# Kernel tuning notes

Hardware: AMD Instinct MI355X
Metric: run time of the kernel (lower is better)

Reference implementation:

```python
import jax, jax.numpy as jnp
import numpy as np

NHEAD, DK, DV, DMODEL, L = 8, 64, 64, 512, 32

def setup_inputs() -> dict:
    key = jax.random.key(0)
    ks = jax.random.split(key, 9)
    B, N = 4, 2048
    s = 1.0 / np.sqrt(DMODEL)
    return {
        "q": jax.random.normal(ks[0], (B, N, DMODEL), jnp.float32),
        "k": jax.random.normal(ks[1], (B, N, DMODEL), jnp.float32),
        "v": jax.random.normal(ks[2], (B, N, DMODEL), jnp.float32),
        "Wq": jax.random.normal(ks[3], (DMODEL, NHEAD * DK), jnp.float32) * s,
        "Wk": jax.random.normal(ks[4], (DMODEL, NHEAD * DK), jnp.float32) * s,
        "Wv": jax.random.normal(ks[5], (DMODEL, NHEAD * DV), jnp.float32) * s,
        "Wfc": jax.random.normal(ks[6], (NHEAD * DV, DMODEL), jnp.float32) * s,
        "ln_g": jnp.ones((DMODEL,), jnp.float32),
        "ln_b": jnp.zeros((DMODEL,), jnp.float32),
    }

def reference(q, k, v, Wq, Wk, Wv, Wfc, ln_g, ln_b):
    B, Nq, _ = q.shape
    residual = q
    # project and split heads: [B, H, N, d]
    qh = (q @ Wq).reshape(B, Nq, NHEAD, DK).transpose(0, 2, 1, 3)
    kh = (k @ Wk).reshape(B, k.shape[1], NHEAD, DK).transpose(0, 2, 1, 3)
    vh = (v @ Wv).reshape(B, v.shape[1], NHEAD, DV).transpose(0, 2, 1, 3)
    # scaled dot-product scores and softmax over keys
    attn = jnp.einsum('bhqd,bhkd->bhqk', qh / jnp.sqrt(jnp.float32(DK)), kh)
    attn = jax.nn.softmax(attn, axis=-1)
    # AWG: keep entries >= l-th largest per row, renormalize
    threshold = jax.lax.top_k(attn, L)[0][..., -1:]  # [B,H,Nq,1]
    W = jnp.where(attn >= threshold, attn, 0.0)
    W_out = W / jnp.sum(W, axis=-1, keepdims=True)
    out = jnp.einsum('bhqk,bhkd->bhqd', W_out, vh)
    out = out.transpose(0, 2, 1, 3).reshape(B, Nq, NHEAD * DV)
    out = out @ Wfc + residual
    # LayerNorm, eps=1e-6
    mu = jnp.mean(out, axis=-1, keepdims=True)
    var = jnp.var(out, axis=-1, keepdims=True)
    return (out - mu) / jnp.sqrt(var + 1e-6) * ln_g + ln_b
```

## Files before the change

### kernel.cpp

```cpp
#include <hip/hip_runtime.h>
#include <hip/hip_fp16.h>

#define BATCH 4
#define NSEQ 2048
#define DMODEL 512
#define NHEAD 8
#define HDIM 64
#define LSEL 32
#define SROWU 2056
#define MAXL 128
#define QROWS 8

typedef __attribute__((ext_vector_type(8))) _Float16 f16x8;
typedef __attribute__((ext_vector_type(4))) float f32x4;

__device__ inline ushort f2h(float x) { __half h = __float2half(x); return *reinterpret_cast<ushort*>(&h); }
__device__ inline uint h2sort(ushort h) { return (h & 0x8000u) ? (uint)(h ^ 0xFFFFu) : (uint)(h | 0x8000u); }
__device__ inline float sort2f(uint su) {
    ushort hb = (su & 0x8000u) ? (ushort)(su ^ 0x8000u) : (ushort)(su ^ 0xFFFFu);
    __half th; *reinterpret_cast<ushort*>(&th) = hb;
    return __half2float(th);
}

__global__ __launch_bounds__(256) void cvtW_kernel(
    const float* __restrict__ Wq, const float* __restrict__ Wk,
    const float* __restrict__ Wv, const float* __restrict__ Wfc,
    ushort* __restrict__ Wt)
{
    const int z = blockIdx.y;
    const float* W = (z == 0) ? Wq : (z == 1) ? Wk : (z == 2) ? Wv : Wfc;
    ushort* O = Wt + (size_t)z * DMODEL * DMODEL;
    const int gt = blockIdx.x * 256 + threadIdx.x;
    const int n = gt & 511;
    const int kc = (gt >> 9) * 16;
    uint pk[8];
#pragma unroll
    for (int i = 0; i < 8; ++i) {
        uint lo = f2h(W[(size_t)(kc + 2 * i) * DMODEL + n]);
        uint hi = f2h(W[(size_t)(kc + 2 * i + 1) * DMODEL + n]);
        pk[i] = lo | (hi << 16);
    }
    uint4 u0 = {pk[0], pk[1], pk[2], pk[3]};
    uint4 u1 = {pk[4], pk[5], pk[6], pk[7]};
    *(uint4*)(O + (size_t)n * DMODEL + kc) = u0;
    *(uint4*)(O + (size_t)n * DMODEL + kc + 8) = u1;
}

template<int MODE>
__global__ __launch_bounds__(256, 2) void hgemm_kernel(
    const float* __restrict__ Fq, const float* __restrict__ Fk, const float* __restrict__ Fv,
    const ushort* __restrict__ A16,
    const ushort* __restrict__ Wt,
    ushort* __restrict__ O0, ushort* __restrict__ O1, ushort* __restrict__ O2,
    float* __restrict__ Ofc)
{
    __shared__ ushort Ah[64][40];
    __shared__ ushort Bh[512][40];

    const int tid = threadIdx.x;
    const int wave = tid >> 6, lane = tid & 63;
    const int lr = lane & 15, lg = lane >> 4;
    const int bm = blockIdx.x * 64;
    const int z = blockIdx.y;

    const float* Af = (MODE == 0) ? (z == 0 ? Fq : z == 1 ? Fk : Fv) : nullptr;
    const ushort* Wz = Wt + (size_t)((MODE == 0) ? z : 3) * (DMODEL * DMODEL);

    f32x4 acc[4][8];
#pragma unroll
    for (int i = 0; i < 4; ++i)
#pragma unroll
        for (int j = 0; j < 8; ++j) acc[i][j] = (f32x4){0.f, 0.f, 0.f, 0.f};

    const int sar = tid >> 2, sak = (tid & 3) * 8;

    for (int k0 = 0; k0 < DMODEL; k0 += 32) {
        __syncthreads();
        if (MODE == 0) {
            float4 fa = *(const float4*)(Af + (size_t)(bm + sar) * DMODEL + k0 + sak);
            float4 fb = *(const float4*)(Af + (size_t)(bm + sar) * DMODEL + k0 + sak + 4);
            uint4 pk;
            pk.x = (uint)f2h(fa.x) | ((uint)f2h(fa.y) << 16);
            pk.y = (uint)f2h(fa.z) | ((uint)f2h(fa.w) << 16);
            pk.z = (uint)f2h(fb.x) | ((uint)f2h(fb.y) << 16);
            pk.w = (uint)f2h(fb.z) | ((uint)f2h(fb.w) << 16);
            *(uint4*)&Ah[sar][sak] = pk;
        } else {
            *(uint4*)&Ah[sar][sak] = *(const uint4*)(A16 + (size_t)(bm + sar) * DMODEL + k0 + sak);
        }
#pragma unroll
        for (int i = 0; i < 8; ++i) {
            int n = sar + 64 * i;
            *(uint4*)&Bh[n][sak] = *(const uint4*)(Wz + (size_t)n * DMODEL + k0 + sak);
        }
        __syncthreads();
        f16x8 af[4];
#pragma unroll
        for (int fr = 0; fr < 4; ++fr) af[fr] = *(const f16x8*)&Ah[fr * 16 + lr][lg * 8];
#pragma unroll
        for (int fc2 = 0; fc2 < 8; ++fc2) {
            f16x8 bf = *(const f16x8*)&Bh[wave * 128 + fc2 * 16 + lr][lg * 8];
#pragma unroll
            for (int fr = 0; fr < 4; ++fr)
                acc[fr][fc2] = __builtin_amdgcn_mfma_f32_16x16x32_f16(af[fr], bf, acc[fr][fc2], 0, 0, 0);
        }
    }

    if (MODE == 1) {
#pragma unroll
        for (int fr = 0; fr < 4; ++fr)
#pragma unroll
            for (int fc2 = 0; fc2 < 8; ++fc2)
#pragma unroll
                for (int r = 0; r < 4; ++r)
                    Ofc[(size_t)(bm + fr * 16 + lg * 4 + r) * DMODEL + wave * 128 + fc2 * 16 + lr] = acc[fr][fc2][r];
        return;
    }

    ushort* O = (z == 0) ? O0 : (z == 1) ? O1 : O2;
    const int b = bm >> 11;
    const int nseq0 = bm & (NSEQ - 1);
    ushort* smw = (ushort*)&Bh[0][0] + wave * (64 * 72);
#pragma unroll
    for (int hp = 0; hp < 2; ++hp) {
        __syncthreads();
#pragma unroll
        for (int f4 = 0; f4 < 4; ++f4) {
            int fc2 = hp * 4 + f4;
            int nl = f4 * 16 + lr;
#pragma unroll
            for (int fr = 0; fr < 4; ++fr)
#pragma unroll
                for (int r = 0; r < 4; ++r)
                    smw[(fr * 16 + lg * 4 + r) * 72 + nl] = f2h(acc[fr][fc2][r]);
        }
        __syncthreads();
        const int h = wave * 2 + hp;
        ushort* obase = O + ((size_t)(b * NHEAD + h) * NSEQ + nseq0) * HDIM;
#pragma unroll
        for (int i = 0; i < 8; ++i) {
            int m = i * 8 + (lane >> 3);
            int dc = (lane & 7) * 8;
            *(uint4*)(obase + (size_t)m * HDIM + dc) = *(const uint4*)(smw + m * 72 + dc);
        }
    }
}

__device__ inline int wave_sum6(int c) {
    int tot = (int)__popcll(__ballot(c & 1));
    tot += (int)__popcll(__ballot(c & 2)) << 1;
    tot += (int)__popcll(__ballot(c & 4)) << 2;
    tot += (int)__popcll(__ballot(c & 8)) << 3;
    tot += (int)__popcll(__ballot(c & 16)) << 4;
    tot += (int)__popcll(__ballot(c & 32)) << 5;
    return tot;
}

__device__ uint full_thr(const ushort* Sr, int lane, uint lo0) {
    uint flo = lo0, fhi = 0xFFFFu;
#pragma unroll 1
    for (int it2 = 0; it2 < 16; ++it2) {
        uint mid = (flo + fhi + 1) >> 1, M = mid << 16;
        int cl = 0;
#pragma unroll
        for (int it = 0; it < 4; ++it) {
            uint4 r4 = *(const uint4*)(Sr + it * 512 + lane * 8);
            cl += ((r4.x << 16) >= M) + ((r4.x & 0xFFFF0000u) >= M);
            cl += ((r4.y << 16) >= M) + ((r4.y & 0xFFFF0000u) >= M);
            cl += ((r4.z << 16) >= M) + ((r4.z & 0xFFFF0000u) >= M);
            cl += ((r4.w << 16) >= M) + ((r4.w & 0xFFFF0000u) >= M);
        }
        bool ge = wave_sum6(cl) >= LSEL;
        flo = ge ? mid : flo;
        fhi = ge ? fhi : mid - 1;
    }
    return flo;
}

__device__ int recount(const ushort* Sr, int lane, uint th) {
    int cs = 0;
#pragma unroll
    for (int it = 0; it < 4; ++it) {
        uint4 r4 = *(const uint4*)(Sr + it * 512 + lane * 8);
        cs += ((r4.x << 16) >= th) + ((r4.x & 0xFFFF0000u) >= th);
        cs += ((r4.y << 16) >= th) + ((r4.y & 0xFFFF0000u) >= th);
        cs += ((r4.z << 16) >= th) + ((r4.z & 0xFFFF0000u) >= th);
        cs += ((r4.w << 16) >= th) + ((r4.w & 0xFFFF0000u) >= th);
    }
    return cs;
}

__device__ float extract_big(const ushort* Sr, int lane, uint th, float Mv,
                             int pre, ushort* li, float* lwp)
{
    const float L2E = 1.4426950408889634f;
    float wp = 0.f;
    int pos = pre;
#pragma unroll
    for (int it = 0; it < 4; ++it) {
        uint4 r4 = *(const uint4*)(Sr + it * 512 + lane * 8);
        uint ib = (uint)(it * 512 + lane * 8);
        uint wds[4] = {r4.x, r4.y, r4.z, r4.w};
#pragma unroll
        for (int c = 0; c < 4; ++c) {
            uint vL = wds[c] << 16, vH = wds[c] & 0xFFFF0000u;
            if (vL >= th) {
                float w = exp2f((sort2f(vL >> 16) - Mv) * L2E);
                if (pos < MAXL) { li[pos] = (ushort)(ib + c * 2); lwp[pos] = w; wp += w; }
                ++pos;
            }
            if (vH >= th) {
                float w = exp2f((sort2f(vH >> 16) - Mv) * L2E);
                if (pos < MAXL) { li[pos] = (ushort)(ib + c * 2 + 1); lwp[pos] = w; wp += w; }
                ++pos;
            }
        }
    }
#pragma unroll
    for (int off = 32; off >= 1; off >>= 1) wp += __shfl_xor(wp, off);
    return wp;
}

__device__ float extract_fast(uint t0, uint t1, uint t2, uint t3,
                              uint th, float Mv, int pre, ushort* li, float* lwp)
{
    const float L2E = 1.4426950408889634f;
    float wp = 0.f;
    uint tt[4] = {t0, t1, t2, t3};
#pragma unroll
    for (int i = 0; i < 4; ++i) {
        if (tt[i] >= th) {
            int pos = pre + i;
            float w = exp2f((sort2f(tt[i] >> 16) - Mv) * L2E);
            if (pos < MAXL) { li[pos] = (ushort)(tt[i] & 0xFFFFu); lwp[pos] = w; wp += w; }
        }
    }
#pragma unroll
    for (int off = 32; off >= 1; off >>= 1) wp += __shfl_xor(wp, off);
    return wp;
}

#define INS5(T0, T1, T2, T3, T4, P) { \
    uint m1_ = min(P, T0); T0 = max(P, T0); \
    uint m2_ = min(m1_, T1); T1 = max(m1_, T1); \
    uint m3_ = min(m2_, T2); T2 = max(m2_, T2); \
    uint m4_ = min(m3_, T3); T3 = max(m3_, T3); \
    T4 = max(m4_, T4); }

__global__ __launch_bounds__(512, 8) void attn_kernel(
    const ushort* __restrict__ qh, const ushort* __restrict__ kh,
    const ushort* __restrict__ vh, ushort* __restrict__ ao)
{
    __shared__ __align__(16) ushort Sbuf[QROWS * SROWU];
    __shared__ ushort lidx[QROWS][MAXL];
    __shared__ float  lw[QROWS][MAXL];

    const int tid = threadIdx.x;
    const int wave = tid >> 6;
    const int lane = tid & 63;
    const int bh = blockIdx.y;
    const int q0 = blockIdx.x * QROWS;
    const int lr = lane & 15;
    const int lg = lane >> 4;

    const ushort* Qb = qh + ((size_t)bh * NSEQ + q0) * HDIM;
    const ushort* Kb = kh + (size_t)bh * NSEQ * HDIM;

    f16x8 qf0 = *(const f16x8*)(Qb + (lr & 7) * HDIM + lg * 8);
    f16x8 qf1 = *(const f16x8*)(Qb + (lr & 7) * HDIM + 32 + lg * 8);

    for (int t = 0; t < 16; ++t) {
        const int k0 = wave * 256 + t * 16;
        const ushort* Kt = Kb + (size_t)k0 * HDIM;
        f16x8 a0 = *(const f16x8*)(Kt + lr * HDIM + lg * 8);
        f16x8 a1 = *(const f16x8*)(Kt + lr * HDIM + 32 + lg * 8);
        f32x4 acc = {0.f, 0.f, 0.f, 0.f};
        acc = __builtin_amdgcn_mfma_f32_16x16x32_f16(a0, qf0, acc, 0, 0, 0);
        acc = __builtin_amdgcn_mfma_f32_16x16x32_f16(a1, qf1, acc, 0, 0, 0);
        if (lr < QROWS) {
            uint2 pk;
            pk.x = h2sort(f2h(acc[0] * 0.125f)) | (h2sort(f2h(acc[1] * 0.125f)) << 16);
            pk.y = h2sort(f2h(acc[2] * 0.125f)) | (h2sort(f2h(acc[3] * 0.125f)) << 16);
            *(uint2*)&Sbuf[lr * SROWU + k0 + lg * 4] = pk;
        }
    }
    __syncthreads();

    const ushort* Vb = vh + (size_t)bh * NSEQ * HDIM;
    const int b = bh >> 3, hh = bh & 7;
    const unsigned long long below = (1ULL << lane) - 1ULL;

    const int qr = wave;
    const ushort* Sr = &Sbuf[qr * SROWU];

    uint a0 = 0, a1 = 0, a2 = 0, a3 = 0, a4 = 0;
#pragma unroll
    for (int it = 0; it < 4; ++it) {
        uint4 ra = *(const uint4*)(Sr + it * 512 + lane * 8);
        uint ib = (uint)(it * 512 + lane * 8);
        uint p;
        p = (ra.x << 16) | (ib + 0); INS5(a0, a1, a2, a3, a4, p);
        p = (ra.x & 0xFFFF0000u) | (ib + 1); INS5(a0, a1, a2, a3, a4, p);
        p = (ra.y << 16) | (ib + 2); INS5(a0, a1, a2, a3, a4, p);
        p = (ra.y & 0xFFFF0000u) | (ib + 3); INS5(a0, a1, a2, a3, a4, p);
        p = (ra.z << 16) | (ib + 4); INS5(a0, a1, a2, a3, a4, p);
        p = (ra.z & 0xFFFF0000u) | (ib + 5); INS5(a0, a1, a2, a3, a4, p);
        p = (ra.w << 16) | (ib + 6); INS5(a0, a1, a2, a3, a4, p);
        p = (ra.w & 0xFFFF0000u) | (ib + 7); INS5(a0, a1, a2, a3, a4, p);
    }

    uint mx = a0;
#pragma unroll
    for (int off = 32; off >= 1; off >>= 1) mx = max(mx, (uint)__shfl_xor((int)mx, off));
    const float Mv = sort2f(mx >> 16);

    uint lo = 0, hi = 0xFFFFu;
#pragma unroll
    for (int it = 0; it < 16; ++it) {
        uint mid = (lo + hi + 1) >> 1, M = mid << 16;
        int c = (a0 >= M) + (a1 >= M) + (a2 >= M) + (a3 >= M);
        int tot = (int)__popcll(__ballot(c & 1)) + ((int)__popcll(__ballot(c & 2)) << 1)
                + ((int)__popcll(__ballot(c & 4)) << 2);
        bool ge = tot >= LSEL;
        lo = ge ? mid : lo;
        hi = ge ? hi : mid - 1;
    }
    uint th = lo << 16;

    const bool miss = __any(a4 >= th);

    int csel;
    if (!miss) {
        csel = (a0 >= th) + (a1 >= th) + (a2 >= th) + (a3 >= th);
    } else {
        int cgt = recount(Sr, lane, th + 0x10000u);
        if (wave_sum6(cgt) >= LSEL) { lo = full_thr(Sr, lane, lo); th = lo << 16; }
        csel = recount(Sr, lane, th);
    }

    int pre = 0, totsel = 0;
#pragma unroll
    for (int bb = 0; bb < 6; ++bb) {
        unsigned long long m = __ballot((csel >> bb) & 1);
        pre += (int)__popcll(m & below) << bb;
        totsel += (int)__popcll(m) << bb;
    }

    const float wsum = miss
        ? extract_big(Sr, lane, th, Mv, pre, &lidx[qr][0], &lw[qr][0])
        : extract_fast(a0, a1, a2, a3, th, Mv, pre, &lidx[qr][0], &lw[qr][0]);

    const int nk = (totsel < MAXL) ? totsel : MAXL;

    asm volatile("s_waitcnt lgkmcnt(0)" ::: "memory");

    const int half = lane >> 5;
    const int dp = lane & 31;
    const __half2* V2 = reinterpret_cast<const __half2*>(Vb);

    float ox = 0.f, oy = 0.f;
    int j = half;
    for (; j + 6 < nk; j += 8) {
        int i0 = lidx[qr][j + 0]; float w0 = lw[qr][j + 0];
        int i1 = lidx[qr][j + 2]; float w1 = lw[qr][j + 2];
        int i2 = lidx[qr][j + 4]; float w2 = lw[qr][j + 4];
        int i3 = lidx[qr][j + 6]; float w3 = lw[qr][j + 6];
        float2 v0 = __half22float2(V2[(size_t)i0 * 32 + dp]);
        float2 v1 = __half22float2(V2[(size_t)i1 * 32 + dp]);
        float2 v2 = __half22float2(V2[(size_t)i2 * 32 + dp]);
        float2 v3 = __half22float2(V2[(size_t)i3 * 32 + dp]);
        ox += w0 * v0.x + w1 * v1.x + w2 * v2.x + w3 * v3.x;
        oy += w0 * v0.y + w1 * v1.y + w2 * v2.y + w3 * v3.y;
    }
    for (; j < nk; j += 2) {
        int i0 = lidx[qr][j]; float w0 = lw[qr][j];
        float2 v0 = __half22float2(V2[(size_t)i0 * 32 + dp]);
        ox += w0 * v0.x; oy += w0 * v0.y;
    }
    ox += __shfl_xor(ox, 32);
    oy += __shfl_xor(oy, 32);

    if (half == 0) {
        const float inv = 1.f / wsum;
        uint opk = (uint)f2h(ox * inv) | ((uint)f2h(oy * inv) << 16);
        *(uint*)(ao + ((size_t)(b * NSEQ) + q0 + qr) * DMODEL + hh * HDIM + dp * 2) = opk;
    }
}

__global__ __launch_bounds__(256) void ln_kernel(
    const float* __restrict__ fcr, const float* __restrict__ resid,
    const float* __restrict__ g, const float* __restrict__ bta, float* __restrict__ out)
{
    const int row = blockIdx.x * 4 + (threadIdx.x >> 6);
    const int lane = threadIdx.x & 63;
    const size_t base = (size_t)row * DMODEL + lane * 8;
    float4 xa = *(const float4*)(fcr + base);
    float4 xb = *(const float4*)(fcr + base + 4);
    float4 ra = *(const float4*)(resid + base);
    float4 rb = *(const float4*)(resid + base + 4);
    xa.x += ra.x; xa.y += ra.y; xa.z += ra.z; xa.w += ra.w;
    xb.x += rb.x; xb.y += rb.y; xb.z += rb.z; xb.w += rb.w;
    float sum = xa.x + xa.y + xa.z + xa.w + xb.x + xb.y + xb.z + xb.w;
    float sq = xa.x * xa.x + xa.y * xa.y + xa.z * xa.z + xa.w * xa.w
             + xb.x * xb.x + xb.y * xb.y + xb.z * xb.z + xb.w * xb.w;
#pragma unroll
    for (int off = 32; off >= 1; off >>= 1) {
        sum += __shfl_xor(sum, off);
        sq += __shfl_xor(sq, off);
    }
    float mean = sum * (1.f / 512.f);
    float var = sq * (1.f / 512.f) - mean * mean;
    float rstd = rsqrtf(var + 1e-6f);
    float4 ga = *(const float4*)(g + lane * 8);
    float4 gb = *(const float4*)(g + lane * 8 + 4);
    float4 ba = *(const float4*)(bta + lane * 8);
    float4 bb = *(const float4*)(bta + lane * 8 + 4);
    float4 oa, ob;
    oa.x = (xa.x - mean) * rstd * ga.x + ba.x;
    oa.y = (xa.y - mean) * rstd * ga.y + ba.y;
    oa.z = (xa.z - mean) * rstd * ga.z + ba.z;
    oa.w = (xa.w - mean) * rstd * ga.w + ba.w;
    ob.x = (xb.x - mean) * rstd * gb.x + bb.x;
    ob.y = (xb.y - mean) * rstd * gb.y + bb.y;
    ob.z = (xb.z - mean) * rstd * gb.z + bb.z;
    ob.w = (xb.w - mean) * rstd * gb.w + bb.w;
    *(float4*)(out + base) = oa;
    *(float4*)(out + base + 4) = ob;
}

extern "C" void kernel_launch(void* const* d_in, const int* in_sizes, int n_in,
                              void* d_out, int out_size, void* d_ws, size_t ws_size,
                              hipStream_t stream)
{
    (void)in_sizes; (void)n_in; (void)out_size; (void)ws_size;

    const float* q   = (const float*)d_in[0];
    const float* k   = (const float*)d_in[1];
    const float* v   = (const float*)d_in[2];
    const float* Wq  = (const float*)d_in[3];
    const float* Wk  = (const float*)d_in[4];
    const float* Wv  = (const float*)d_in[5];
    const float* Wfc = (const float*)d_in[6];
    const float* g   = (const float*)d_in[7];
    const float* b   = (const float*)d_in[8];
    float* out = (float*)d_out;

    const size_t SZ = (size_t)BATCH * NSEQ * DMODEL;
    const size_t WSZ = (size_t)DMODEL * DMODEL;
    ushort* Wt = (ushort*)d_ws;
    ushort* qh = Wt + 4 * WSZ;
    ushort* kh = qh + SZ;
    ushort* vh = kh + SZ;
    ushort* ao = vh + SZ;
    float* fc_raw = (float*)qh;

    cvtW_kernel<<<dim3(64, 4), 256, 0, stream>>>(Wq, Wk, Wv, Wfc, Wt);
    hgemm_kernel<0><<<dim3(128, 3), 256, 0, stream>>>(q, k, v, nullptr, Wt, qh, kh, vh, nullptr);
    attn_kernel<<<dim3(NSEQ / QROWS, BATCH * NHEAD), 512, 0, stream>>>(qh, kh, vh, ao);
    hgemm_kernel<1><<<dim3(128, 1), 256, 0, stream>>>(nullptr, nullptr, nullptr, ao, Wt, nullptr, nullptr, nullptr, fc_raw);
    ln_kernel<<<(BATCH * NSEQ) / 4, 256, 0, stream>>>(fc_raw, q, g, b, out);
}
```

Measured before the change: 390.1 us.

## Restructure attention top-k selection and add separate fp16 input conversion pass

```diff
diff --git a/kernel.cpp b/kernel.cpp
--- a/kernel.cpp
+++ b/kernel.cpp
@@ -8,18 +8,40 @@
 #define HDIM 64
 #define LSEL 32
 #define SROWU 2056
-#define MAXL 128
-#define QROWS 8
+#define MAXL 64
+#define QROWS 16
+#define CSTRIDE 165
 
 typedef __attribute__((ext_vector_type(8))) _Float16 f16x8;
 typedef __attribute__((ext_vector_type(4))) float f32x4;
+typedef unsigned long long ull;
 
 __device__ inline ushort f2h(float x) { __half h = __float2half(x); return *reinterpret_cast<ushort*>(&h); }
-__device__ inline uint h2sort(ushort h) { return (h & 0x8000u) ? (uint)(h ^ 0xFFFFu) : (uint)(h | 0x8000u); }
+__device__ inline float h16f(ushort u) { __half t; *reinterpret_cast<ushort*>(&t) = u; return __half2float(t); }
 __device__ inline float sort2f(uint su) {
     ushort hb = (su & 0x8000u) ? (ushort)(su ^ 0x8000u) : (ushort)(su ^ 0xFFFFu);
-    __half th; *reinterpret_cast<ushort*>(&th) = hb;
-    return __half2float(th);
+    return h16f(hb);
+}
+__device__ inline uint sm2(uint w) {
+    uint s = (w >> 15) & 0x00010001u;
+    uint m = s * 0x7FFFu;
+    return w ^ (m | 0x80008000u);
+}
+
+__global__ __launch_bounds__(256) void cvtA_kernel(
+    const float* __restrict__ q, const float* __restrict__ k, const float* __restrict__ v,
+    ushort* __restrict__ q16, ushort* __restrict__ k16, ushort* __restrict__ v16)
+{
+    const int z = blockIdx.y;
+    const float* src = (z == 0) ? q : (z == 1) ? k : v;
+    ushort* dst = (z == 0) ? q16 : (z == 1) ? k16 : v16;
+    const size_t base = (size_t)blockIdx.x * 2048 + threadIdx.x * 4;
+    float4 fa = *(const float4*)(src + base);
+    float4 fb = *(const float4*)(src + base + 1024);
+    ushort4 ha = {f2h(fa.x), f2h(fa.y), f2h(fa.z), f2h(fa.w)};
+    ushort4 hb = {f2h(fb.x), f2h(fb.y), f2h(fb.z), f2h(fb.w)};
+    *(ushort4*)(dst + base) = ha;
+    *(ushort4*)(dst + base + 1024) = hb;
 }
 
 __global__ __launch_bounds__(256) void cvtW_kernel(
@@ -48,8 +70,7 @@
 
 template<int MODE>
 __global__ __launch_bounds__(256, 2) void hgemm_kernel(
-    const float* __restrict__ Fq, const float* __restrict__ Fk, const float* __restrict__ Fv,
-    const ushort* __restrict__ A16,
+    const ushort* __restrict__ A0, const ushort* __restrict__ A1, const ushort* __restrict__ A2,
     const ushort* __restrict__ Wt,
     ushort* __restrict__ O0, ushort* __restrict__ O1, ushort* __restrict__ O2,
     float* __restrict__ Ofc)
@@ -63,7 +84,7 @@
     const int bm = blockIdx.x * 64;
     const int z = blockIdx.y;
 
-    const float* Af = (MODE == 0) ? (z == 0 ? Fq : z == 1 ? Fk : Fv) : nullptr;
+    const ushort* A16 = (MODE == 0) ? (z == 0 ? A0 : z == 1 ? A1 : A2) : A0;
     const ushort* Wz = Wt + (size_t)((MODE == 0) ? z : 3) * (DMODEL * DMODEL);
 
     f32x4 acc[4][8];
@@ -76,18 +97,7 @@
 
     for (int k0 = 0; k0 < DMODEL; k0 += 32) {
         __syncthreads();
-        if (MODE == 0) {
-            float4 fa = *(const float4*)(Af + (size_t)(bm + sar) * DMODEL + k0 + sak);
-            float4 fb = *(const float4*)(Af + (size_t)(bm + sar) * DMODEL + k0 + sak + 4);
-            uint4 pk;
-            pk.x = (uint)f2h(fa.x) | ((uint)f2h(fa.y) << 16);
-            pk.y = (uint)f2h(fa.z) | ((uint)f2h(fa.w) << 16);
-            pk.z = (uint)f2h(fb.x) | ((uint)f2h(fb.y) << 16);
-            pk.w = (uint)f2h(fb.z) | ((uint)f2h(fb.w) << 16);
-            *(uint4*)&Ah[sar][sak] = pk;
-        } else {
-            *(uint4*)&Ah[sar][sak] = *(const uint4*)(A16 + (size_t)(bm + sar) * DMODEL + k0 + sak);
-        }
+        *(uint4*)&Ah[sar][sak] = *(const uint4*)(A16 + (size_t)(bm + sar) * DMODEL + k0 + sak);
 #pragma unroll
         for (int i = 0; i < 8; ++i) {
             int n = sar + 64 * i;
@@ -117,6 +127,7 @@
         return;
     }
 
+    const float osc = (z == 0) ? 0.125f : 1.0f;
     ushort* O = (z == 0) ? O0 : (z == 1) ? O1 : O2;
     const int b = bm >> 11;
     const int nseq0 = bm & (NSEQ - 1);
@@ -132,7 +143,7 @@
             for (int fr = 0; fr < 4; ++fr)
 #pragma unroll
                 for (int r = 0; r < 4; ++r)
-                    smw[(fr * 16 + lg * 4 + r) * 72 + nl] = f2h(acc[fr][fc2][r]);
+                    smw[(fr * 16 + lg * 4 + r) * 72 + nl] = f2h(acc[fr][fc2][r] * osc);
         }
         __syncthreads();
         const int h = wave * 2 + hp;
@@ -191,7 +202,7 @@
 }
 
 __device__ float extract_big(const ushort* Sr, int lane, uint th, float Mv,
-                             int pre, ushort* li, float* lwp)
+                             int pre, uint* selrow)
 {
     const float L2E = 1.4426950408889634f;
     float wp = 0.f;
@@ -205,34 +216,15 @@
         for (int c = 0; c < 4; ++c) {
             uint vL = wds[c] << 16, vH = wds[c] & 0xFFFF0000u;
             if (vL >= th) {
-                float w = exp2f((sort2f(vL >> 16) - Mv) * L2E);
-                if (pos < MAXL) { li[pos] = (ushort)(ib + c * 2); lwp[pos] = w; wp += w; }
+                ushort w16 = f2h(exp2f((sort2f(vL >> 16) - Mv) * L2E));
+                if (pos < MAXL) { selrow[pos] = ((uint)w16 << 16) | (ib + c * 2); wp += h16f(w16); }
                 ++pos;
             }
             if (vH >= th) {
-                float w = exp2f((sort2f(vH >> 16) - Mv) * L2E);
-                if (pos < MAXL) { li[pos] = (ushort)(ib + c * 2 + 1); lwp[pos] = w; wp += w; }
+                ushort w16 = f2h(exp2f((sort2f(vH >> 16) - Mv) * L2E));
+                if (pos < MAXL) { selrow[pos] = ((uint)w16 << 16) | (ib + c * 2 + 1); wp += h16f(w16); }
                 ++pos;
             }
-        }
-    }
-#pragma unroll
-    for (int off = 32; off >= 1; off >>= 1) wp += __shfl_xor(wp, off);
-    return wp;
-}
-
-__device__ float extract_fast(uint t0, uint t1, uint t2, uint t3,
-                              uint th, float Mv, int pre, ushort* li, float* lwp)
-{
-    const float L2E = 1.4426950408889634f;
-    float wp = 0.f;
-    uint tt[4] = {t0, t1, t2, t3};
-#pragma unroll
-    for (int i = 0; i < 4; ++i) {
-        if (tt[i] >= th) {
-            int pos = pre + i;
-            float w = exp2f((sort2f(tt[i] >> 16) - Mv) * L2E);
-            if (pos < MAXL) { li[pos] = (ushort)(tt[i] & 0xFFFFu); lwp[pos] = w; wp += w; }
         }
     }
 #pragma unroll
@@ -247,13 +239,13 @@
     uint m4_ = min(m3_, T3); T3 = max(m3_, T3); \
     T4 = max(m4_, T4); }
 
-__global__ __launch_bounds__(512, 8) void attn_kernel(
+__global__ __launch_bounds__(512, 4) void attn_kernel(
     const ushort* __restrict__ qh, const ushort* __restrict__ kh,
     const ushort* __restrict__ vh, ushort* __restrict__ ao)
 {
     __shared__ __align__(16) ushort Sbuf[QROWS * SROWU];
-    __shared__ ushort lidx[QROWS][MAXL];
-    __shared__ float  lw[QROWS][MAXL];
+    __shared__ uint cand[QROWS * CSTRIDE];
+    __shared__ __align__(16) uint sel[QROWS][MAXL];
 
     const int tid = threadIdx.x;
     const int wave = tid >> 6;
@@ -262,129 +254,209 @@
     const int q0 = blockIdx.x * QROWS;
     const int lr = lane & 15;
     const int lg = lane >> 4;
+    const float L2E = 1.4426950408889634f;
 
     const ushort* Qb = qh + ((size_t)bh * NSEQ + q0) * HDIM;
     const ushort* Kb = kh + (size_t)bh * NSEQ * HDIM;
 
-    f16x8 qf0 = *(const f16x8*)(Qb + (lr & 7) * HDIM + lg * 8);
-    f16x8 qf1 = *(const f16x8*)(Qb + (lr & 7) * HDIM + 32 + lg * 8);
-
+    f16x8 qf0 = *(const f16x8*)(Qb + lr * HDIM + lg * 8);
+    f16x8 qf1 = *(const f16x8*)(Qb + lr * HDIM + 32 + lg * 8);
+
+    uint u00 = 0, u01 = 0, u02 = 0, u03 = 0, u04 = 0;
+    uint u10 = 0, u11 = 0, u12 = 0, u13 = 0, u14 = 0;
+    uint u20 = 0, u21 = 0, u22 = 0, u23 = 0, u24 = 0;
+    uint u30 = 0, u31 = 0, u32 = 0, u33 = 0, u34 = 0;
+
+    const int kwbase = wave * 256;
+    const ushort* Kt0 = Kb + (size_t)kwbase * HDIM;
+    f16x8 a0 = *(const f16x8*)(Kt0 + lr * HDIM + lg * 8);
+    f16x8 a1 = *(const f16x8*)(Kt0 + lr * HDIM + 32 + lg * 8);
+
+#pragma unroll
     for (int t = 0; t < 16; ++t) {
-        const int k0 = wave * 256 + t * 16;
-        const ushort* Kt = Kb + (size_t)k0 * HDIM;
-        f16x8 a0 = *(const f16x8*)(Kt + lr * HDIM + lg * 8);
-        f16x8 a1 = *(const f16x8*)(Kt + lr * HDIM + 32 + lg * 8);
+        f16x8 n0 = a0, n1 = a1;
+        if (t < 15) {
+            const ushort* Kn = Kb + (size_t)(kwbase + (t + 1) * 16) * HDIM;
+            n0 = *(const f16x8*)(Kn + lr * HDIM + lg * 8);
+            n1 = *(const f16x8*)(Kn + lr * HDIM + 32 + lg * 8);
+        }
         f32x4 acc = {0.f, 0.f, 0.f, 0.f};
         acc = __builtin_amdgcn_mfma_f32_16x16x32_f16(a0, qf0, acc, 0, 0, 0);
         acc = __builtin_amdgcn_mfma_f32_16x16x32_f16(a1, qf1, acc, 0, 0, 0);
-        if (lr < QROWS) {
-            uint2 pk;
-            pk.x = h2sort(f2h(acc[0] * 0.125f)) | (h2sort(f2h(acc[1] * 0.125f)) << 16);
-            pk.y = h2sort(f2h(acc[2] * 0.125f)) | (h2sort(f2h(acc[3] * 0.125f)) << 16);
-            *(uint2*)&Sbuf[lr * SROWU + k0 + lg * 4] = pk;
-        }
+        const uint col = (uint)(kwbase + t * 16 + lg * 4);
+        uint w0 = (uint)f2h(acc[0]) | ((uint)f2h(acc[1]) << 16);
+        uint w1 = (uint)f2h(acc[2]) | ((uint)f2h(acc[3]) << 16);
+        w0 = sm2(w0); w1 = sm2(w1);
+        uint2 pk = {w0, w1};
+        *(uint2*)&Sbuf[lr * SROWU + col] = pk;
+        uint p;
+        p = (w0 << 16) | col;               INS5(u00, u01, u02, u03, u04, p);
+        p = (w0 & 0xFFFF0000u) | (col + 1); INS5(u10, u11, u12, u13, u14, p);
+        p = (w1 << 16) | (col + 2);         INS5(u20, u21, u22, u23, u24, p);
+        p = (w1 & 0xFFFF0000u) | (col + 3); INS5(u30, u31, u32, u33, u34, p);
+        a0 = n0; a1 = n1;
+    }
+
+    INS5(u00, u01, u02, u03, u04, u10); INS5(u00, u01, u02, u03, u04, u11);
+    INS5(u00, u01, u02, u03, u04, u12); INS5(u00, u01, u02, u03, u04, u13);
+    INS5(u00, u01, u02, u03, u04, u14);
+    INS5(u00, u01, u02, u03, u04, u20); INS5(u00, u01, u02, u03, u04, u21);
+    INS5(u00, u01, u02, u03, u04, u22); INS5(u00, u01, u02, u03, u04, u23);
+    INS5(u00, u01, u02, u03, u04, u24);
+    INS5(u00, u01, u02, u03, u04, u30); INS5(u00, u01, u02, u03, u04, u31);
+    INS5(u00, u01, u02, u03, u04, u32); INS5(u00, u01, u02, u03, u04, u33);
+    INS5(u00, u01, u02, u03, u04, u34);
+
+    {
+        const int sidx = wave * 4 + lg;
+        const int cb = lr * CSTRIDE + sidx;
+        cand[cb +   0] = u00;
+        cand[cb +  33] = u01;
+        cand[cb +  66] = u02;
+        cand[cb +  99] = u03;
+        cand[cb + 132] = u04;
     }
     __syncthreads();
 
-    const ushort* Vb = vh + (size_t)bh * NSEQ * HDIM;
+    const int halfid = lane >> 5;
+    const int s = lane & 31;
+    const int qrA = wave * 2, qrB = qrA + 1;
+    const int qrMy = qrA + halfid;
     const int b = bh >> 3, hh = bh & 7;
-    const unsigned long long below = (1ULL << lane) - 1ULL;
-
-    const int qr = wave;
-    const ushort* Sr = &Sbuf[qr * SROWU];
-
-    uint a0 = 0, a1 = 0, a2 = 0, a3 = 0, a4 = 0;
-#pragma unroll
-    for (int it = 0; it < 4; ++it) {
-        uint4 ra = *(const uint4*)(Sr + it * 512 + lane * 8);
-        uint ib = (uint)(it * 512 + lane * 8);
-        uint p;
-        p = (ra.x << 16) | (ib + 0); INS5(a0, a1, a2, a3, a4, p);
-        p = (ra.x & 0xFFFF0000u) | (ib + 1); INS5(a0, a1, a2, a3, a4, p);
-        p = (ra.y << 16) | (ib + 2); INS5(a0, a1, a2, a3, a4, p);
-        p = (ra.y & 0xFFFF0000u) | (ib + 3); INS5(a0, a1, a2, a3, a4, p);
-        p = (ra.z << 16) | (ib + 4); INS5(a0, a1, a2, a3, a4, p);
-        p = (ra.z & 0xFFFF0000u) | (ib + 5); INS5(a0, a1, a2, a3, a4, p);
-        p = (ra.w << 16) | (ib + 6); INS5(a0, a1, a2, a3, a4, p);
-        p = (ra.w & 0xFFFF0000u) | (ib + 7); INS5(a0, a1, a2, a3, a4, p);
-    }
-
-    uint mx = a0;
-#pragma unroll
-    for (int off = 32; off >= 1; off >>= 1) mx = max(mx, (uint)__shfl_xor((int)mx, off));
+
+    uint c0, c1, c2, c3, c4;
+    {
+        const int cb = qrMy * CSTRIDE + s;
+        c0 = cand[cb]; c1 = cand[cb + 33]; c2 = cand[cb + 66];
+        c3 = cand[cb + 99]; c4 = cand[cb + 132];
+    }
+
+    uint mx = c0;
+#pragma unroll
+    for (int off = 1; off <= 16; off <<= 1) mx = max(mx, (uint)__shfl_xor((int)mx, off));
     const float Mv = sort2f(mx >> 16);
 
     uint lo = 0, hi = 0xFFFFu;
 #pragma unroll
     for (int it = 0; it < 16; ++it) {
         uint mid = (lo + hi + 1) >> 1, M = mid << 16;
-        int c = (a0 >= M) + (a1 >= M) + (a2 >= M) + (a3 >= M);
-        int tot = (int)__popcll(__ballot(c & 1)) + ((int)__popcll(__ballot(c & 2)) << 1)
-                + ((int)__popcll(__ballot(c & 4)) << 2);
-        bool ge = tot >= LSEL;
+        int cnt = (c0 >= M) + (c1 >= M) + (c2 >= M) + (c3 >= M) + (c4 >= M);
+        ull m0 = __ballot(cnt & 1), m1 = __ballot(cnt & 2), m2 = __ballot(cnt & 4);
+        int tA = (int)__popcll(m0 & 0xFFFFFFFFull) + 2 * (int)__popcll(m1 & 0xFFFFFFFFull)
+               + 4 * (int)__popcll(m2 & 0xFFFFFFFFull);
+        int tB = (int)__popcll(m0 >> 32) + 2 * (int)__popcll(m1 >> 32) + 4 * (int)__popcll(m2 >> 32);
+        bool ge = (halfid ? tB : tA) >= LSEL;
         lo = ge ? mid : lo;
         hi = ge ? hi : mid - 1;
     }
     uint th = lo << 16;
 
-    const bool miss = __any(a4 >= th);
-
-    int csel;
-    if (!miss) {
-        csel = (a0 >= th) + (a1 >= th) + (a2 >= th) + (a3 >= th);
-    } else {
-        int cgt = recount(Sr, lane, th + 0x10000u);
-        if (wave_sum6(cgt) >= LSEL) { lo = full_thr(Sr, lane, lo); th = lo << 16; }
-        csel = recount(Sr, lane, th);
-    }
-
-    int pre = 0, totsel = 0;
-#pragma unroll
-    for (int bb = 0; bb < 6; ++bb) {
-        unsigned long long m = __ballot((csel >> bb) & 1);
-        pre += (int)__popcll(m & below) << bb;
-        totsel += (int)__popcll(m) << bb;
-    }
-
-    const float wsum = miss
-        ? extract_big(Sr, lane, th, Mv, pre, &lidx[qr][0], &lw[qr][0])
-        : extract_fast(a0, a1, a2, a3, th, Mv, pre, &lidx[qr][0], &lw[qr][0]);
-
-    const int nk = (totsel < MAXL) ? totsel : MAXL;
+    const float MvA = __shfl(Mv, 0), MvB = __shfl(Mv, 32);
+    const uint loA = (uint)__shfl((int)lo, 0), loB = (uint)__shfl((int)lo, 32);
+
+    ull mm = __ballot(c4 >= th);
+    const bool missA = (mm & 0xFFFFFFFFull) != 0ull;
+    const bool missB = (mm >> 32) != 0ull;
+    const bool myMiss = halfid ? missB : missA;
+
+    float wsMy = 1.f;
+    int nkMy = 0;
+
+    if (!myMiss) {
+        int cs = (c0 >= th) + (c1 >= th) + (c2 >= th) + (c3 >= th);
+        ull HB = halfid ? 0xFFFFFFFF00000000ull : 0x00000000FFFFFFFFull;
+        ull below = ((1ull << lane) - 1ull) & HB;
+        int pre = 0, tot = 0;
+#pragma unroll
+        for (int bb = 0; bb < 3; ++bb) {
+            ull m = __ballot((cs >> bb) & 1);
+            pre += (int)__popcll(m & below) << bb;
+            tot += (int)__popcll(m & HB) << bb;
+        }
+        float wp = 0.f;
+        uint cc0 = c0, cc1 = c1, cc2 = c2, cc3 = c3;
+#pragma unroll
+        for (int i = 0; i < 4; ++i) {
+            uint ci = (i == 0) ? cc0 : (i == 1) ? cc1 : (i == 2) ? cc2 : cc3;
+            if (ci >= th) {
+                ushort w16 = f2h(exp2f((sort2f(ci >> 16) - Mv) * L2E));
+                int pos = pre + i;
+                if (pos < MAXL) { sel[qrMy][pos] = ((uint)w16 << 16) | (ci & 0xFFFFu); wp += h16f(w16); }
+            }
+        }
+#pragma unroll
+        for (int off = 1; off <= 16; off <<= 1) wp += __shfl_xor(wp, off);
+        wsMy = wp;
+        nkMy = (tot < MAXL) ? tot : MAXL;
+    }
+
+    if (missA) {
+        const ushort* Sr = &Sbuf[qrA * SROWU];
+        uint ft = full_thr(Sr, lane, loA);
+        uint thv = ft << 16;
+        int cs = recount(Sr, lane, thv);
+        ull below64 = (1ull << lane) - 1ull;
+        int preS = 0, totS = 0;
+#pragma unroll
+        for (int bb = 0; bb < 6; ++bb) {
+            ull m = __ballot((cs >> bb) & 1);
+            preS += (int)__popcll(m & below64) << bb;
+            totS += (int)__popcll(m) << bb;
+        }
+        float wa = extract_big(Sr, lane, thv, MvA, preS, &sel[qrA][0]);
+        if (halfid == 0) { wsMy = wa; nkMy = (totS < MAXL) ? totS : MAXL; }
+    }
+    if (missB) {
+        const ushort* Sr = &Sbuf[qrB * SROWU];
+        uint ft = full_thr(Sr, lane, loB);
+        uint thv = ft << 16;
+        int cs = recount(Sr, lane, thv);
+        ull below64 = (1ull << lane) - 1ull;
+        int preS = 0, totS = 0;
+#pragma unroll
+        for (int bb = 0; bb < 6; ++bb) {
+            ull m = __ballot((cs >> bb) & 1);
+            preS += (int)__popcll(m & below64) << bb;
+            totS += (int)__popcll(m) << bb;
+        }
+        float wb = extract_big(Sr, lane, thv, MvB, preS, &sel[qrB][0]);
+        if (halfid == 1) { wsMy = wb; nkMy = (totS < MAXL) ? totS : MAXL; }
+    }
 
     asm volatile("s_waitcnt lgkmcnt(0)" ::: "memory");
 
-    const int half = lane >> 5;
+    const __half2* V2 = reinterpret_cast<const __half2*>(vh + (size_t)bh * NSEQ * HDIM);
     const int dp = lane & 31;
-    const __half2* V2 = reinterpret_cast<const __half2*>(Vb);
+    const uint* selp = &sel[qrMy][0];
 
     float ox = 0.f, oy = 0.f;
-    int j = half;
-    for (; j + 6 < nk; j += 8) {
-        int i0 = lidx[qr][j + 0]; float w0 = lw[qr][j + 0];
-        int i1 = lidx[qr][j + 2]; float w1 = lw[qr][j + 2];
-        int i2 = lidx[qr][j + 4]; float w2 = lw[qr][j + 4];
-        int i3 = lidx[qr][j + 6]; float w3 = lw[qr][j + 6];
-        float2 v0 = __half22float2(V2[(size_t)i0 * 32 + dp]);
-        float2 v1 = __half22float2(V2[(size_t)i1 * 32 + dp]);
-        float2 v2 = __half22float2(V2[(size_t)i2 * 32 + dp]);
-        float2 v3 = __half22float2(V2[(size_t)i3 * 32 + dp]);
-        ox += w0 * v0.x + w1 * v1.x + w2 * v2.x + w3 * v3.x;
-        oy += w0 * v0.y + w1 * v1.y + w2 * v2.y + w3 * v3.y;
-    }
-    for (; j < nk; j += 2) {
-        int i0 = lidx[qr][j]; float w0 = lw[qr][j];
-        float2 v0 = __half22float2(V2[(size_t)i0 * 32 + dp]);
-        ox += w0 * v0.x; oy += w0 * v0.y;
-    }
-    ox += __shfl_xor(ox, 32);
-    oy += __shfl_xor(oy, 32);
-
-    if (half == 0) {
-        const float inv = 1.f / wsum;
-        uint opk = (uint)f2h(ox * inv) | ((uint)f2h(oy * inv) << 16);
-        *(uint*)(ao + ((size_t)(b * NSEQ) + q0 + qr) * DMODEL + hh * HDIM + dp * 2) = opk;
-    }
+    int j = 0;
+    for (; j + 8 <= nkMy; j += 8) {
+        uint e[8];
+        *(uint4*)&e[0] = *(const uint4*)(selp + j);
+        *(uint4*)&e[4] = *(const uint4*)(selp + j + 4);
+        float2 vv[8];
+        float ww[8];
+#pragma unroll
+        for (int i2 = 0; i2 < 8; ++i2) {
+            int idx = (int)(e[i2] & 0xFFFFu);
+            ww[i2] = h16f((ushort)(e[i2] >> 16));
+            vv[i2] = __half22float2(V2[(size_t)idx * 32 + dp]);
+        }
+#pragma unroll
+        for (int i2 = 0; i2 < 8; ++i2) { ox += ww[i2] * vv[i2].x; oy += ww[i2] * vv[i2].y; }
+    }
+    for (; j < nkMy; ++j) {
+        uint e = selp[j];
+        int idx = (int)(e & 0xFFFFu);
+        float w = h16f((ushort)(e >> 16));
+        float2 v0 = __half22float2(V2[(size_t)idx * 32 + dp]);
+        ox += w * v0.x; oy += w * v0.y;
+    }
+
+    const float inv = 1.f / wsMy;
+    uint opk = (uint)f2h(ox * inv) | ((uint)f2h(oy * inv) << 16);
+    *(uint*)(ao + ((size_t)(b * NSEQ) + q0 + qrMy) * DMODEL + hh * HDIM + dp * 2) = opk;
 }
 
 __global__ __launch_bounds__(256) void ln_kernel(
@@ -447,16 +519,21 @@
 
     const size_t SZ = (size_t)BATCH * NSEQ * DMODEL;
     const size_t WSZ = (size_t)DMODEL * DMODEL;
-    ushort* Wt = (ushort*)d_ws;
-    ushort* qh = Wt + 4 * WSZ;
-    ushort* kh = qh + SZ;
-    ushort* vh = kh + SZ;
-    ushort* ao = vh + SZ;
-    float* fc_raw = (float*)qh;
-
+    ushort* w16 = (ushort*)d_ws;
+    ushort* q16 = w16;
+    ushort* k16 = w16 + SZ;
+    ushort* v16 = w16 + 2 * SZ;
+    ushort* Wt  = w16 + 3 * SZ;
+    ushort* qh  = Wt + 4 * WSZ;
+    ushort* kh  = qh + SZ;
+    ushort* vh  = kh + SZ;
+    ushort* ao  = vh + SZ;
+    float* fc_raw = (float*)d_ws;
+
+    cvtA_kernel<<<dim3(2048, 3), 256, 0, stream>>>(q, k, v, q16, k16, v16);
     cvtW_kernel<<<dim3(64, 4), 256, 0, stream>>>(Wq, Wk, Wv, Wfc, Wt);
-    hgemm_kernel<0><<<dim3(128, 3), 256, 0, stream>>>(q, k, v, nullptr, Wt, qh, kh, vh, nullptr);
+    hgemm_kernel<0><<<dim3(128, 3), 256, 0, stream>>>(q16, k16, v16, Wt, qh, kh, vh, nullptr);
     attn_kernel<<<dim3(NSEQ / QROWS, BATCH * NHEAD), 512, 0, stream>>>(qh, kh, vh, ao);
-    hgemm_kernel<1><<<dim3(128, 1), 256, 0, stream>>>(nullptr, nullptr, nullptr, ao, Wt, nullptr, nullptr, nullptr, fc_raw);
+    hgemm_kernel<1><<<dim3(128, 1), 256, 0, stream>>>(ao, nullptr, nullptr, Wt, nullptr, nullptr, nullptr, fc_raw);
     ln_kernel<<<(BATCH * NSEQ) / 4, 256, 0, stream>>>(fc_raw, q, g, b, out);
 }
```

New measurement: 324.7 us. 1.2x faster.
